# Performance work log

Measured on AMD Instinct MI355X. Metric: run time of the kernel, lower is better.

## Reference

```python
import jax, jax.numpy as jnp
import numpy as np

B, T, D, H = 4, 2048, 1024, 16
HD = D // H  # 64
NEG = -np.finfo(np.float32).max


def setup_inputs() -> dict:
    key = jax.random.key(0)
    ks = jax.random.split(key, 9)
    s = 1.0 / np.sqrt(D)
    return {
        "x": jax.random.normal(ks[0], (B, T, D), jnp.float32),
        "wq": jax.random.normal(ks[1], (D, D), jnp.float32) * s,
        "bq": jax.random.normal(ks[2], (D,), jnp.float32) * 0.02,
        "wk": jax.random.normal(ks[3], (D, D), jnp.float32) * s,
        "bk": jax.random.normal(ks[4], (D,), jnp.float32) * 0.02,
        "wv": jax.random.normal(ks[5], (D, D), jnp.float32) * s,
        "bv": jax.random.normal(ks[6], (D,), jnp.float32) * 0.02,
        "wo": jax.random.normal(ks[7], (D, D), jnp.float32) * s,
        "bo": jax.random.normal(ks[8], (D,), jnp.float32) * 0.02,
    }


def reference(x, wq, bq, wk, bk, wv, bv, wo, bo):
    b, t, d = x.shape
    # separate Q, K, V projections, reshape to (B, H, T, HD)
    def proj(w, bias):
        y = x @ w + bias
        return y.reshape(b, t, H, HD).transpose(0, 2, 1, 3)
    q = proj(wq, bq)
    k = proj(wk, bk)
    v = proj(wv, bv)
    scale = 1.0 / np.sqrt(HD).astype(np.float32)
    scores = jnp.einsum("bhqd,bhkd->bhqk", q, k) * scale  # (B,H,T,T)
    # causal mask: -max_float on strictly upper triangle (matches source)
    mask = jnp.triu(jnp.full((t, t), NEG, jnp.float32), k=1)
    attn = jax.nn.softmax(scores + mask, axis=-1)
    out = jnp.einsum("bhqk,bhkd->bhqd", attn, v)
    out = out.transpose(0, 2, 1, 3).reshape(b, t, d)
    return out @ wo + bo
```

## Files before the change

### kernel.cpp

```cpp
#include <hip/hip_runtime.h>

typedef __bf16 bf16x8 __attribute__((ext_vector_type(8)));
typedef float f32x4 __attribute__((ext_vector_type(4)));

#define B_ 4
#define T_ 2048
#define D_ 1024
#define H_ 16
#define HD_ 64
#define M_ 8192
#define QSCALE 0.1803368801111204f

__device__ __forceinline__ ushort f2b(float f) {
  union { float f; unsigned u; } v; v.f = f;
  unsigned u = v.u;
  return (ushort)((u + 0x7FFFu + ((u >> 16) & 1u)) >> 16);
}

__device__ __forceinline__ unsigned pkbf(float a, float b) {
  union { float f; unsigned u; } va, vb; va.f = a; vb.f = b;
  return __builtin_amdgcn_perm(vb.u + 0x8000u, va.u + 0x8000u, 0x07060302u);
}

__global__ __launch_bounds__(256) void cast_x_kernel(const float* __restrict__ x,
                                                     ushort* __restrict__ xb) {
  int idx = blockIdx.x * 256 + threadIdx.x;
  float4 v = ((const float4*)x)[idx];
  ushort4 o;
  o.x = f2b(v.x); o.y = f2b(v.y); o.z = f2b(v.z); o.w = f2b(v.w);
  ((ushort4*)xb)[idx] = o;
}

__global__ __launch_bounds__(256) void transpose_w_kernel(
    const float* __restrict__ wq, const float* __restrict__ wk,
    const float* __restrict__ wv, const float* __restrict__ wo,
    ushort* __restrict__ wt_qkv, ushort* __restrict__ wt_o) {
  __shared__ float tile[32][33];
  int z = blockIdx.z;
  const float* src = (z == 0) ? wq : (z == 1) ? wk : (z == 2) ? wv : wo;
  ushort* dst = (z < 3) ? (wt_qkv + (size_t)z * D_ * D_) : wt_o;
  int n0 = blockIdx.x * 32, k0 = blockIdx.y * 32;
  int tx = threadIdx.x & 31, ty = threadIdx.x >> 5;
  for (int i = 0; i < 4; i++) {
    int r = ty + i * 8;
    tile[r][tx] = src[(size_t)(k0 + r) * D_ + n0 + tx];
  }
  __syncthreads();
  for (int i = 0; i < 4; i++) {
    int r = ty + i * 8;
    dst[(size_t)(n0 + r) * D_ + k0 + tx] = f2b(tile[tx][r]);
  }
}

__global__ __launch_bounds__(256) void gemm_kernel(
    const ushort* __restrict__ A, const ushort* __restrict__ Bt, int mode,
    const float* __restrict__ bias_q, const float* __restrict__ bias_k,
    const float* __restrict__ bias_v,
    ushort* __restrict__ qb, ushort* __restrict__ kb, ushort* __restrict__ vtb,
    float* __restrict__ outf) {
  __shared__ ushort As[2][128][64];
  __shared__ ushort Bs[2][128][64];
  int tid = threadIdx.x;
  int wave = tid >> 6, lane = tid & 63, lrow = lane >> 4, lcol = lane & 15;
  int m0 = blockIdx.y * 128, n0 = blockIdx.x * 128;
  int wm = (wave & 1) * 64, wn = (wave >> 1) * 64;

  int rb = tid >> 3;
  int dc = tid & 7;
  int scv = dc ^ (rb & 7);
  const ushort* aBase = A + (size_t)(m0 + rb) * D_ + scv * 8;
  const ushort* bBase = Bt + (size_t)(n0 + rb) * D_ + scv * 8;

  f32x4 zero = {0.f, 0.f, 0.f, 0.f};
  f32x4 acc[4][4];
  for (int i = 0; i < 4; i++)
    for (int j = 0; j < 4; j++) acc[i][j] = zero;

  int swz = lcol & 7;

  {
    uint4 a0 = *(const uint4*)(aBase);
    uint4 a1 = *(const uint4*)(aBase + (size_t)32 * D_);
    uint4 a2 = *(const uint4*)(aBase + (size_t)64 * D_);
    uint4 a3 = *(const uint4*)(aBase + (size_t)96 * D_);
    uint4 b0 = *(const uint4*)(bBase);
    uint4 b1 = *(const uint4*)(bBase + (size_t)32 * D_);
    uint4 b2 = *(const uint4*)(bBase + (size_t)64 * D_);
    uint4 b3 = *(const uint4*)(bBase + (size_t)96 * D_);
    *(uint4*)&As[0][rb][dc * 8] = a0;
    *(uint4*)&As[0][rb + 32][dc * 8] = a1;
    *(uint4*)&As[0][rb + 64][dc * 8] = a2;
    *(uint4*)&As[0][rb + 96][dc * 8] = a3;
    *(uint4*)&Bs[0][rb][dc * 8] = b0;
    *(uint4*)&Bs[0][rb + 32][dc * 8] = b1;
    *(uint4*)&Bs[0][rb + 64][dc * 8] = b2;
    *(uint4*)&Bs[0][rb + 96][dc * 8] = b3;
  }

  for (int k0 = 0; k0 < D_; k0 += 64) {
    int cur = (k0 >> 6) & 1, nxt = cur ^ 1;
    int kn = (k0 + 64 < D_) ? k0 + 64 : k0;
    __syncthreads();

    uint4 a0 = *(const uint4*)(aBase + kn);
    uint4 a1 = *(const uint4*)(aBase + (size_t)32 * D_ + kn);
    uint4 a2 = *(const uint4*)(aBase + (size_t)64 * D_ + kn);
    uint4 a3 = *(const uint4*)(aBase + (size_t)96 * D_ + kn);
    uint4 b0 = *(const uint4*)(bBase + kn);
    uint4 b1 = *(const uint4*)(bBase + (size_t)32 * D_ + kn);
    uint4 b2 = *(const uint4*)(bBase + (size_t)64 * D_ + kn);
    uint4 b3 = *(const uint4*)(bBase + (size_t)96 * D_ + kn);

    for (int ks = 0; ks < 2; ks++) {
      bf16x8 af[4], bf[4];
      int ch = ((ks * 4 + lrow) ^ swz) * 8;
      for (int mt = 0; mt < 4; mt++)
        af[mt] = *(const bf16x8*)&As[cur][wm + mt * 16 + lcol][ch];
      for (int nt = 0; nt < 4; nt++)
        bf[nt] = *(const bf16x8*)&Bs[cur][wn + nt * 16 + lcol][ch];
      for (int mt = 0; mt < 4; mt++)
        for (int nt = 0; nt < 4; nt++)
          acc[mt][nt] = __builtin_amdgcn_mfma_f32_16x16x32_bf16(
              af[mt], bf[nt], acc[mt][nt], 0, 0, 0);
    }

    if (k0 + 64 < D_) {
      *(uint4*)&As[nxt][rb][dc * 8] = a0;
      *(uint4*)&As[nxt][rb + 32][dc * 8] = a1;
      *(uint4*)&As[nxt][rb + 64][dc * 8] = a2;
      *(uint4*)&As[nxt][rb + 96][dc * 8] = a3;
      *(uint4*)&Bs[nxt][rb][dc * 8] = b0;
      *(uint4*)&Bs[nxt][rb + 32][dc * 8] = b1;
      *(uint4*)&Bs[nxt][rb + 64][dc * 8] = b2;
      *(uint4*)&Bs[nxt][rb + 96][dc * 8] = b3;
    }
  }

  if (mode == 0) {
    int proj = n0 >> 10;
    const float* bias = (proj == 0) ? bias_q : (proj == 1) ? bias_k : bias_v;
    for (int mt = 0; mt < 4; mt++) {
      int gm0 = m0 + wm + mt * 16 + lrow * 4;
      int b = gm0 >> 11, tp = gm0 & 2047;
      for (int nt = 0; nt < 4; nt++) {
        int gn = n0 + wn + nt * 16 + lcol;
        int inner = gn & 1023;
        int h = inner >> 6, hd = inner & 63;
        float bv = bias[inner];
        if (proj == 0) {
          size_t base = ((size_t)(b * H_ + h) * T_ + tp) * HD_ + hd;
          for (int r = 0; r < 4; r++)
            qb[base + (size_t)r * HD_] = f2b((acc[mt][nt][r] + bv) * QSCALE);
        } else if (proj == 1) {
          size_t base = ((size_t)(b * H_ + h) * T_ + tp) * HD_ + hd;
          for (int r = 0; r < 4; r++)
            kb[base + (size_t)r * HD_] = f2b(acc[mt][nt][r] + bv);
        } else {
          ushort4 pk;
          pk.x = f2b(acc[mt][nt][0] + bv);
          pk.y = f2b(acc[mt][nt][1] + bv);
          pk.z = f2b(acc[mt][nt][2] + bv);
          pk.w = f2b(acc[mt][nt][3] + bv);
          *(ushort4*)&vtb[((size_t)(b * H_ + h) * HD_ + hd) * T_ + tp] = pk;
        }
      }
    }
  } else {
    for (int mt = 0; mt < 4; mt++) {
      int gm0 = m0 + wm + mt * 16 + lrow * 4;
      for (int nt = 0; nt < 4; nt++) {
        int gn = n0 + wn + nt * 16 + lcol;
        float bv = bias_q[gn];
        for (int r = 0; r < 4; r++)
          outf[(size_t)(gm0 + r) * D_ + gn] = acc[mt][nt][r] + bv;
      }
    }
  }
}

__global__ __launch_bounds__(256) void flash_kernel(
    const ushort* __restrict__ qb, const ushort* __restrict__ kb,
    const ushort* __restrict__ vtb, ushort* __restrict__ ob) {
  __shared__ ushort Ks[64][80];
  __shared__ ushort Vs[64][80];
  __shared__ ushort Ps[4][16][80];
  int tid = threadIdx.x;
  int wave = tid >> 6, lane = tid & 63, lrow = lane >> 4, lcol = lane & 15;
  int p = blockIdx.x;
  int bh = blockIdx.y;
  int b = bh >> 4, h = bh & 15;
  const ushort* qh = qb + (size_t)bh * T_ * HD_;
  const ushort* kh = kb + (size_t)bh * T_ * HD_;
  const ushort* vh = vtb + (size_t)bh * HD_ * T_;

  int r0 = tid >> 3, cb0 = (tid & 7) * 8;
  uint4 kr0 = *(const uint4*)&kh[(size_t)r0 * HD_ + cb0];
  uint4 kr1 = *(const uint4*)&kh[(size_t)(r0 + 32) * HD_ + cb0];
  uint4 vr0 = *(const uint4*)&vh[(size_t)r0 * T_ + cb0];
  uint4 vr1 = *(const uint4*)&vh[(size_t)(r0 + 32) * T_ + cb0];

  f32x4 zero = {0.f, 0.f, 0.f, 0.f};

  for (int pass = 0; pass < 2; pass++) {
    int qtile = pass ? p : (31 - p);
    int q0w = qtile * 64 + wave * 16;
    bf16x8 qf[2];
    for (int ks = 0; ks < 2; ks++)
      qf[ks] = *(const bf16x8*)&qh[(size_t)(q0w + lcol) * HD_ + ks * 32 + lrow * 8];

    float m_run = -1e30f, l_run = 0.f;
    f32x4 accO[4];
    for (int mt = 0; mt < 4; mt++) accO[mt] = zero;

    for (int j = 0; j <= qtile; j++) {
      __syncthreads();
      *(uint4*)&Ks[r0][cb0] = kr0;
      *(uint4*)&Ks[r0 + 32][cb0] = kr1;
      *(uint4*)&Vs[r0][cb0] = vr0;
      *(uint4*)&Vs[r0 + 32][cb0] = vr1;
      __syncthreads();

      if (j < qtile || pass == 0) {
        int jn = (j < qtile) ? j + 1 : 0;
        kr0 = *(const uint4*)&kh[(size_t)(jn * 64 + r0) * HD_ + cb0];
        kr1 = *(const uint4*)&kh[(size_t)(jn * 64 + r0 + 32) * HD_ + cb0];
        vr0 = *(const uint4*)&vh[(size_t)r0 * T_ + jn * 64 + cb0];
        vr1 = *(const uint4*)&vh[(size_t)(r0 + 32) * T_ + jn * 64 + cb0];
      }

      f32x4 st[4];
      for (int mt = 0; mt < 4; mt++) st[mt] = zero;
      for (int ks = 0; ks < 2; ks++)
        for (int mt = 0; mt < 4; mt++) {
          bf16x8 kf = *(const bf16x8*)&Ks[mt * 16 + lcol][ks * 32 + lrow * 8];
          st[mt] = __builtin_amdgcn_mfma_f32_16x16x32_bf16(kf, qf[ks], st[mt], 0, 0, 0);
        }

      if (j == qtile) {
        int q_g = q0w + lcol;
        for (int mt = 0; mt < 4; mt++)
          for (int r = 0; r < 4; r++) {
            int kv_g = j * 64 + mt * 16 + lrow * 4 + r;
            if (kv_g > q_g) st[mt][r] = -1e30f;
          }
      }

      float mx = fmaxf(
          fmaxf(fmaxf(fmaxf(st[0][0], st[0][1]), fmaxf(st[0][2], st[0][3])),
                fmaxf(fmaxf(st[1][0], st[1][1]), fmaxf(st[1][2], st[1][3]))),
          fmaxf(fmaxf(fmaxf(st[2][0], st[2][1]), fmaxf(st[2][2], st[2][3])),
                fmaxf(fmaxf(st[3][0], st[3][1]), fmaxf(st[3][2], st[3][3]))));
      mx = fmaxf(mx, __shfl_xor(mx, 16));
      mx = fmaxf(mx, __shfl_xor(mx, 32));
      float mn = fmaxf(m_run, mx);
      float alpha = __builtin_amdgcn_exp2f(m_run - mn);
      m_run = mn;
      float rs = 0.f;
      for (int mt = 0; mt < 4; mt++)
        for (int r = 0; r < 4; r++) {
          float pv = __builtin_amdgcn_exp2f(st[mt][r] - mn);
          st[mt][r] = pv;
          rs += pv;
        }
      rs += __shfl_xor(rs, 16);
      rs += __shfl_xor(rs, 32);
      l_run = l_run * alpha + rs;

      for (int mt = 0; mt < 4; mt++) {
        uint2 pk;
        pk.x = pkbf(st[mt][0], st[mt][1]);
        pk.y = pkbf(st[mt][2], st[mt][3]);
        *(uint2*)&Ps[wave][lcol][mt * 16 + lrow * 4] = pk;
      }

      for (int mt = 0; mt < 4; mt++)
        for (int r = 0; r < 4; r++) accO[mt][r] *= alpha;

      for (int ks = 0; ks < 2; ks++) {
        bf16x8 pf = *(const bf16x8*)&Ps[wave][lcol][ks * 32 + lrow * 8];
        for (int mt = 0; mt < 4; mt++) {
          bf16x8 vf = *(const bf16x8*)&Vs[mt * 16 + lcol][ks * 32 + lrow * 8];
          accO[mt] = __builtin_amdgcn_mfma_f32_16x16x32_bf16(vf, pf, accO[mt], 0, 0, 0);
        }
      }
    }

    float linv = 1.f / l_run;
    int t = q0w + lcol;
    size_t base = ((size_t)b * T_ + t) * D_ + h * HD_;
    for (int mt = 0; mt < 4; mt++) {
      uint2 pk;
      pk.x = pkbf(accO[mt][0] * linv, accO[mt][1] * linv);
      pk.y = pkbf(accO[mt][2] * linv, accO[mt][3] * linv);
      *(uint2*)&ob[base + mt * 16 + lrow * 4] = pk;
    }
  }
}

extern "C" void kernel_launch(void* const* d_in, const int* in_sizes, int n_in,
                              void* d_out, int out_size, void* d_ws, size_t ws_size,
                              hipStream_t stream) {
  (void)in_sizes; (void)n_in; (void)out_size; (void)ws_size;
  const float* x  = (const float*)d_in[0];
  const float* wq = (const float*)d_in[1];
  const float* bq = (const float*)d_in[2];
  const float* wk = (const float*)d_in[3];
  const float* bk = (const float*)d_in[4];
  const float* wv = (const float*)d_in[5];
  const float* bv = (const float*)d_in[6];
  const float* wo = (const float*)d_in[7];
  const float* bo = (const float*)d_in[8];
  float* out = (float*)d_out;

  char* ws = (char*)d_ws;
  ushort* xb     = (ushort*)(ws);
  ushort* wt_qkv = (ushort*)(ws + 16777216);
  ushort* wt_o   = (ushort*)(ws + 23068672);
  ushort* qb     = (ushort*)(ws + 25165824);
  ushort* kb     = (ushort*)(ws + 41943040);
  ushort* vtb    = (ushort*)(ws + 58720256);
  ushort* ob     = (ushort*)(ws + 75497472);

  cast_x_kernel<<<8192, 256, 0, stream>>>(x, xb);
  transpose_w_kernel<<<dim3(32, 32, 4), 256, 0, stream>>>(wq, wk, wv, wo, wt_qkv, wt_o);
  gemm_kernel<<<dim3(24, 64), 256, 0, stream>>>(xb, wt_qkv, 0, bq, bk, bv, qb, kb, vtb, nullptr);
  flash_kernel<<<dim3(16, 64), 256, 0, stream>>>(qb, kb, vtb, ob);
  gemm_kernel<<<dim3(8, 64), 256, 0, stream>>>(ob, wt_o, 1, bo, nullptr, nullptr,
                                               nullptr, nullptr, nullptr, out);
}
```

Before: 280.0 us.

## Process 128-query tiles per flash block and compute row sums via MFMA

The flash attention block now handles 128 query rows, 32 per wave in two 16-row groups, so each K/V tile loaded into shared memory is reused for twice as many queries. The launch grid drops to 8x64 blocks with causal pairing adjusted to 16 tiles. The softmax row sum is now accumulated by an extra MFMA against a ones-column matrix instead of shuffle reductions. In exchange there are fewer blocks, which lowers occupancy and parallelism, and more registers per thread.

```diff
diff --git a/kernel.cpp b/kernel.cpp
--- a/kernel.cpp
+++ b/kernel.cpp
@@ -183,7 +183,7 @@
     const ushort* __restrict__ vtb, ushort* __restrict__ ob) {
   __shared__ ushort Ks[64][80];
   __shared__ ushort Vs[64][80];
-  __shared__ ushort Ps[4][16][80];
+  __shared__ ushort Ps[4][32][80];
   int tid = threadIdx.x;
   int wave = tid >> 6, lane = tid & 63, lrow = lane >> 4, lcol = lane & 15;
   int p = blockIdx.x;
@@ -199,20 +199,33 @@
   uint4 vr0 = *(const uint4*)&vh[(size_t)r0 * T_ + cb0];
   uint4 vr1 = *(const uint4*)&vh[(size_t)(r0 + 32) * T_ + cb0];
 
+  bf16x8 af1;
+  {
+    __bf16 ov = (__bf16)((lcol == 0) ? 1.0f : 0.0f);
+    for (int i = 0; i < 8; i++) af1[i] = ov;
+  }
+
   f32x4 zero = {0.f, 0.f, 0.f, 0.f};
 
   for (int pass = 0; pass < 2; pass++) {
-    int qtile = pass ? p : (31 - p);
-    int q0w = qtile * 64 + wave * 16;
-    bf16x8 qf[2];
-    for (int ks = 0; ks < 2; ks++)
-      qf[ks] = *(const bf16x8*)&qh[(size_t)(q0w + lcol) * HD_ + ks * 32 + lrow * 8];
-
-    float m_run = -1e30f, l_run = 0.f;
-    f32x4 accO[4];
-    for (int mt = 0; mt < 4; mt++) accO[mt] = zero;
-
-    for (int j = 0; j <= qtile; j++) {
+    int qtile = pass ? p : (15 - p);
+    int q0w = qtile * 128 + wave * 32;
+    bf16x8 qf[2][2];
+    for (int qg = 0; qg < 2; qg++)
+      for (int ks = 0; ks < 2; ks++)
+        qf[qg][ks] = *(const bf16x8*)&qh[(size_t)(q0w + qg * 16 + lcol) * HD_ +
+                                         ks * 32 + lrow * 8];
+
+    float m_run[2] = {-1e30f, -1e30f};
+    f32x4 accO[2][4];
+    f32x4 accI[2];
+    for (int qg = 0; qg < 2; qg++) {
+      accI[qg] = zero;
+      for (int mt = 0; mt < 4; mt++) accO[qg][mt] = zero;
+    }
+
+    int jmax = 2 * qtile + 1;
+    for (int j = 0; j <= jmax; j++) {
       __syncthreads();
       *(uint4*)&Ks[r0][cb0] = kr0;
       *(uint4*)&Ks[r0 + 32][cb0] = kr1;
@@ -220,79 +233,84 @@
       *(uint4*)&Vs[r0 + 32][cb0] = vr1;
       __syncthreads();
 
-      if (j < qtile || pass == 0) {
-        int jn = (j < qtile) ? j + 1 : 0;
+      if (j < jmax || pass == 0) {
+        int jn = (j < jmax) ? j + 1 : 0;
         kr0 = *(const uint4*)&kh[(size_t)(jn * 64 + r0) * HD_ + cb0];
         kr1 = *(const uint4*)&kh[(size_t)(jn * 64 + r0 + 32) * HD_ + cb0];
         vr0 = *(const uint4*)&vh[(size_t)r0 * T_ + jn * 64 + cb0];
         vr1 = *(const uint4*)&vh[(size_t)(r0 + 32) * T_ + jn * 64 + cb0];
       }
 
-      f32x4 st[4];
-      for (int mt = 0; mt < 4; mt++) st[mt] = zero;
+      f32x4 st[4][2];
+      for (int mt = 0; mt < 4; mt++)
+        for (int qg = 0; qg < 2; qg++) st[mt][qg] = zero;
       for (int ks = 0; ks < 2; ks++)
         for (int mt = 0; mt < 4; mt++) {
           bf16x8 kf = *(const bf16x8*)&Ks[mt * 16 + lcol][ks * 32 + lrow * 8];
-          st[mt] = __builtin_amdgcn_mfma_f32_16x16x32_bf16(kf, qf[ks], st[mt], 0, 0, 0);
-        }
-
-      if (j == qtile) {
-        int q_g = q0w + lcol;
+          st[mt][0] = __builtin_amdgcn_mfma_f32_16x16x32_bf16(kf, qf[0][ks], st[mt][0], 0, 0, 0);
+          st[mt][1] = __builtin_amdgcn_mfma_f32_16x16x32_bf16(kf, qf[1][ks], st[mt][1], 0, 0, 0);
+        }
+
+      if (j >= 2 * qtile) {
+        for (int qg = 0; qg < 2; qg++) {
+          int q_g = q0w + qg * 16 + lcol;
+          for (int mt = 0; mt < 4; mt++)
+            for (int r = 0; r < 4; r++) {
+              int kv_g = j * 64 + mt * 16 + lrow * 4 + r;
+              if (kv_g > q_g) st[mt][qg][r] = -1e30f;
+            }
+        }
+      }
+
+      for (int qg = 0; qg < 2; qg++) {
+        float mx = fmaxf(
+            fmaxf(fmaxf(fmaxf(st[0][qg][0], st[0][qg][1]), fmaxf(st[0][qg][2], st[0][qg][3])),
+                  fmaxf(fmaxf(st[1][qg][0], st[1][qg][1]), fmaxf(st[1][qg][2], st[1][qg][3]))),
+            fmaxf(fmaxf(fmaxf(st[2][qg][0], st[2][qg][1]), fmaxf(st[2][qg][2], st[2][qg][3])),
+                  fmaxf(fmaxf(st[3][qg][0], st[3][qg][1]), fmaxf(st[3][qg][2], st[3][qg][3]))));
+        mx = fmaxf(mx, __shfl_xor(mx, 16));
+        mx = fmaxf(mx, __shfl_xor(mx, 32));
+        float mn = fmaxf(m_run[qg], mx);
+        float alpha = __builtin_amdgcn_exp2f(m_run[qg] - mn);
+        m_run[qg] = mn;
         for (int mt = 0; mt < 4; mt++)
-          for (int r = 0; r < 4; r++) {
-            int kv_g = j * 64 + mt * 16 + lrow * 4 + r;
-            if (kv_g > q_g) st[mt][r] = -1e30f;
-          }
-      }
-
-      float mx = fmaxf(
-          fmaxf(fmaxf(fmaxf(st[0][0], st[0][1]), fmaxf(st[0][2], st[0][3])),
-                fmaxf(fmaxf(st[1][0], st[1][1]), fmaxf(st[1][2], st[1][3]))),
-          fmaxf(fmaxf(fmaxf(st[2][0], st[2][1]), fmaxf(st[2][2], st[2][3])),
-                fmaxf(fmaxf(st[3][0], st[3][1]), fmaxf(st[3][2], st[3][3]))));
-      mx = fmaxf(mx, __shfl_xor(mx, 16));
-      mx = fmaxf(mx, __shfl_xor(mx, 32));
-      float mn = fmaxf(m_run, mx);
-      float alpha = __builtin_amdgcn_exp2f(m_run - mn);
-      m_run = mn;
-      float rs = 0.f;
-      for (int mt = 0; mt < 4; mt++)
-        for (int r = 0; r < 4; r++) {
-          float pv = __builtin_amdgcn_exp2f(st[mt][r] - mn);
-          st[mt][r] = pv;
-          rs += pv;
-        }
-      rs += __shfl_xor(rs, 16);
-      rs += __shfl_xor(rs, 32);
-      l_run = l_run * alpha + rs;
-
+          for (int r = 0; r < 4; r++)
+            st[mt][qg][r] = __builtin_amdgcn_exp2f(st[mt][qg][r] - mn);
+        accI[qg][0] *= alpha;
+        for (int mt = 0; mt < 4; mt++)
+          for (int r = 0; r < 4; r++) accO[qg][mt][r] *= alpha;
+        for (int mt = 0; mt < 4; mt++) {
+          uint2 pk;
+          pk.x = pkbf(st[mt][qg][0], st[mt][qg][1]);
+          pk.y = pkbf(st[mt][qg][2], st[mt][qg][3]);
+          *(uint2*)&Ps[wave][qg * 16 + lcol][mt * 16 + lrow * 4] = pk;
+        }
+      }
+
+      for (int ks = 0; ks < 2; ks++) {
+        bf16x8 pf0 = *(const bf16x8*)&Ps[wave][lcol][ks * 32 + lrow * 8];
+        bf16x8 pf1 = *(const bf16x8*)&Ps[wave][16 + lcol][ks * 32 + lrow * 8];
+        accI[0] = __builtin_amdgcn_mfma_f32_16x16x32_bf16(af1, pf0, accI[0], 0, 0, 0);
+        accI[1] = __builtin_amdgcn_mfma_f32_16x16x32_bf16(af1, pf1, accI[1], 0, 0, 0);
+        for (int mt = 0; mt < 4; mt++) {
+          bf16x8 vf = *(const bf16x8*)&Vs[mt * 16 + lcol][ks * 32 + lrow * 8];
+          accO[0][mt] = __builtin_amdgcn_mfma_f32_16x16x32_bf16(vf, pf0, accO[0][mt], 0, 0, 0);
+          accO[1][mt] = __builtin_amdgcn_mfma_f32_16x16x32_bf16(vf, pf1, accO[1][mt], 0, 0, 0);
+        }
+      }
+    }
+
+    for (int qg = 0; qg < 2; qg++) {
+      float lsum = __shfl(accI[qg][0], lcol);
+      float linv = 1.f / lsum;
+      int t = q0w + qg * 16 + lcol;
+      size_t base = ((size_t)b * T_ + t) * D_ + h * HD_;
       for (int mt = 0; mt < 4; mt++) {
         uint2 pk;
-        pk.x = pkbf(st[mt][0], st[mt][1]);
-        pk.y = pkbf(st[mt][2], st[mt][3]);
-        *(uint2*)&Ps[wave][lcol][mt * 16 + lrow * 4] = pk;
-      }
-
-      for (int mt = 0; mt < 4; mt++)
-        for (int r = 0; r < 4; r++) accO[mt][r] *= alpha;
-
-      for (int ks = 0; ks < 2; ks++) {
-        bf16x8 pf = *(const bf16x8*)&Ps[wave][lcol][ks * 32 + lrow * 8];
-        for (int mt = 0; mt < 4; mt++) {
-          bf16x8 vf = *(const bf16x8*)&Vs[mt * 16 + lcol][ks * 32 + lrow * 8];
-          accO[mt] = __builtin_amdgcn_mfma_f32_16x16x32_bf16(vf, pf, accO[mt], 0, 0, 0);
-        }
-      }
-    }
-
-    float linv = 1.f / l_run;
-    int t = q0w + lcol;
-    size_t base = ((size_t)b * T_ + t) * D_ + h * HD_;
-    for (int mt = 0; mt < 4; mt++) {
-      uint2 pk;
-      pk.x = pkbf(accO[mt][0] * linv, accO[mt][1] * linv);
-      pk.y = pkbf(accO[mt][2] * linv, accO[mt][3] * linv);
-      *(uint2*)&ob[base + mt * 16 + lrow * 4] = pk;
+        pk.x = pkbf(accO[qg][mt][0] * linv, accO[qg][mt][1] * linv);
+        pk.y = pkbf(accO[qg][mt][2] * linv, accO[qg][mt][3] * linv);
+        *(uint2*)&ob[base + mt * 16 + lrow * 4] = pk;
+      }
     }
   }
 }
@@ -324,7 +342,7 @@
   cast_x_kernel<<<8192, 256, 0, stream>>>(x, xb);
   transpose_w_kernel<<<dim3(32, 32, 4), 256, 0, stream>>>(wq, wk, wv, wo, wt_qkv, wt_o);
   gemm_kernel<<<dim3(24, 64), 256, 0, stream>>>(xb, wt_qkv, 0, bq, bk, bv, qb, kb, vtb, nullptr);
-  flash_kernel<<<dim3(16, 64), 256, 0, stream>>>(qb, kb, vtb, ob);
+  flash_kernel<<<dim3(8, 64), 256, 0, stream>>>(qb, kb, vtb, ob);
   gemm_kernel<<<dim3(8, 64), 256, 0, stream>>>(ob, wt_o, 1, bo, nullptr, nullptr,
                                                nullptr, nullptr, nullptr, out);
 }
```

Result: no change. 276.7 us (-1.2%).
